# Kernel tuning notes

Measured on AMD Instinct MI355X. Metric: run time of the kernel, lower is better.

Reference implementation:

```python
import jax, jax.numpy as jnp
import numpy as np

B, S, M, H = 4, 512, 128, 768
KEY_SIZE, VALUE_SIZE = 30000, 10000


def setup_inputs() -> dict:
    key = jax.random.key(0)
    k1, k2, k3, k4, k5, k6 = jax.random.split(key, 6)
    return {
        "word_seq": jax.random.randint(k1, (B, M), 0, KEY_SIZE),
        "hidden_state": jax.random.normal(k2, (B, S, H), dtype=jnp.float32),
        "label_value_matrix": jax.random.randint(k3, (B, S, M), 0, VALUE_SIZE),
        "word_mask_metrix": jax.random.uniform(k4, (B, S, M), dtype=jnp.float32),
        "key_table": jax.random.normal(k5, (KEY_SIZE, H), dtype=jnp.float32) * 0.02,
        "value_table": jax.random.normal(k6, (VALUE_SIZE, H), dtype=jnp.float32) * 0.02,
    }


def reference(word_seq, hidden_state, label_value_matrix, word_mask_metrix,
              key_table, value_table):
    temper = jnp.asarray(H, hidden_state.dtype) ** 0.5
    emb_a = key_table[word_seq]                      # [B, M, H]
    # u[b,s,m] = <hidden_state[b,s], emb_a[b,m]> / sqrt(H)
    u = jnp.einsum('bsh,bmh->bsm', hidden_state, emb_a) / temper
    mask = jnp.clip(word_mask_metrix, 0.0, 1.0)      # [B, S, M]
    delta_exp_u = jnp.exp(u) * mask                  # masked unnormalized attn
    p = delta_exp_u / (jnp.sum(delta_exp_u, axis=2, keepdims=True) + 1e-10)
    emb_c = value_table[label_value_matrix]          # [B, S, M, H]
    # o[b,s,h] = sum_m p[b,s,m] * emb_c[b,s,m,h]
    o = jnp.einsum('bsm,bsmh->bsh', p, emb_c)
    return o
```

## Files before the change

### kernel.cpp

```cpp
#include <hip/hip_runtime.h>
#include <hip/hip_bf16.h>


constexpr int B = 4, S = 512, M = 128, H = 768;
constexpr int C4 = H / 4;
constexpr int KEY_SIZE = 30000, VALUE_SIZE = 10000;

constexpr int VT_N = VALUE_SIZE * H;
constexpr int KA_N = B * M * H;
constexpr int HS_N = B * S * H;
constexpr int U_N  = B * S * M;

constexpr size_t VT_BYTES = (size_t)VT_N * 2;
constexpr size_t KA_BYTES = (size_t)KA_N * 2;
constexpr size_t HS_BYTES = (size_t)HS_N * 2;
constexpr size_t U_BYTES  = (size_t)U_N  * 4;
constexpr size_t WS_NEEDED = VT_BYTES + KA_BYTES + HS_BYTES + U_BYTES;

constexpr int VT_V4 = VT_N / 4, KA_V4 = KA_N / 4, HS_V4 = HS_N / 4;
constexpr int CONV_TOTAL = VT_V4 + KA_V4 + HS_V4;

typedef short          bf16x8  __attribute__((ext_vector_type(8)));
typedef float          floatx4 __attribute__((ext_vector_type(4)));
typedef unsigned short ushort8v __attribute__((ext_vector_type(8)));

__device__ inline unsigned short f2bf(float f) {
    __hip_bfloat16 h = __float2bfloat16(f);
    return *reinterpret_cast<unsigned short*>(&h);
}
__device__ inline float bf2f(unsigned short u) {
    return __uint_as_float((unsigned)u << 16);
}
__device__ inline ushort4 f4_to_bf4(float4 f) {
    ushort4 u; u.x = f2bf(f.x); u.y = f2bf(f.y); u.z = f2bf(f.z); u.w = f2bf(f.w);
    return u;
}

__global__ __launch_bounds__(256) void convert_kernel(
    const float* __restrict__ vt, const float* __restrict__ kt,
    const float* __restrict__ hs, const int* __restrict__ wseq,
    unsigned short* __restrict__ vt_bf, unsigned short* __restrict__ ka_bf,
    unsigned short* __restrict__ hs_bf)
{
    int i = blockIdx.x * 256 + threadIdx.x;
    if (i < VT_V4) {
        ((ushort4*)vt_bf)[i] = f4_to_bf4(((const float4*)vt)[i]);
    } else if (i < VT_V4 + KA_V4) {
        int j   = i - VT_V4;
        int c   = j % (H / 4);
        int row = j / (H / 4);
        int src = wseq[row];
        float4 f = ((const float4*)(kt + (size_t)src * H))[c];
        ((ushort4*)ka_bf)[j] = f4_to_bf4(f);
    } else if (i < CONV_TOTAL) {
        int j = i - VT_V4 - KA_V4;
        ((ushort4*)hs_bf)[j] = f4_to_bf4(((const float4*)hs)[j]);
    }
}

__global__ __launch_bounds__(256) void phaseA_kernel(
    const unsigned short* __restrict__ hs_bf,
    const unsigned short* __restrict__ ka_bf,
    float* __restrict__ u_ws)
{
    const int lane = threadIdx.x & 63;
    const int wave = threadIdx.x >> 6;
    const int tile = blockIdx.x * 4 + wave;
    const int b    = tile >> 8;
    const int r    = tile & 255;
    const int s0   = (r >> 3) << 4;
    const int m0   = (r & 7) << 4;
    const int l15  = lane & 15;
    const int quad = lane >> 4;

    const unsigned short* arow = hs_bf + (size_t)(b * S + s0 + l15) * H + quad * 8;
    const unsigned short* brow = ka_bf + (size_t)(b * M + m0 + l15) * H + quad * 8;

    floatx4 acc = {0.f, 0.f, 0.f, 0.f};
    #pragma unroll 4
    for (int k = 0; k < H; k += 32) {
        bf16x8 af = *(const bf16x8*)(arow + k);
        bf16x8 bf = *(const bf16x8*)(brow + k);
        acc = __builtin_amdgcn_mfma_f32_16x16x32_bf16(af, bf, acc, 0, 0, 0);
    }
    float* up = u_ws + (size_t)(b * S + s0 + quad * 4) * M + m0 + l15;
    up[0 * M] = acc[0];
    up[1 * M] = acc[1];
    up[2 * M] = acc[2];
    up[3 * M] = acc[3];
}

__global__ __launch_bounds__(192) void gather_kernel(
    const float* __restrict__ u_ws,
    const int*   __restrict__ lvm,
    const float* __restrict__ mask,
    const unsigned short* __restrict__ vt_bf,
    float*       __restrict__ out)
{
    const int bs = blockIdx.x;
    const int t  = threadIdx.x;
    const int p  = t / 96;
    const int c  = t - p * 96;

    __shared__ float delta_s[M];
    __shared__ int   row_s[M];
    __shared__ float merge_s[8][100];
    __shared__ float dsum_s;

    const float inv_temper = rsqrtf((float)H);
    if (t < M) {
        float u  = u_ws[(size_t)bs * M + t];
        float mk = mask[(size_t)bs * M + t];
        mk = fminf(fmaxf(mk, 0.f), 1.f);
        delta_s[t] = __expf(u * inv_temper) * mk;
        row_s[t]   = lvm[(size_t)bs * M + t];
    }
    __syncthreads();

    if (t < 64) {
        float d = delta_s[t] + delta_s[t + 64];
        #pragma unroll
        for (int off = 1; off < 64; off <<= 1) d += __shfl_xor(d, off);
        if (t == 0) dsum_s = d + 1e-10f;
    }

    float a0 = 0.f, a1 = 0.f, a2 = 0.f, a3 = 0.f;
    float a4 = 0.f, a5 = 0.f, a6 = 0.f, a7 = 0.f;

    const unsigned short* base = vt_bf + c * 8;
    #pragma unroll 8
    for (int m = p; m < M; m += 2) {
        const float pm = delta_s[m];
        ushort8v v = *(const ushort8v*)(base + (size_t)row_s[m] * H);
        a0 += pm * bf2f(v[0]);
        a1 += pm * bf2f(v[1]);
        a2 += pm * bf2f(v[2]);
        a3 += pm * bf2f(v[3]);
        a4 += pm * bf2f(v[4]);
        a5 += pm * bf2f(v[5]);
        a6 += pm * bf2f(v[6]);
        a7 += pm * bf2f(v[7]);
    }

    if (p == 1) {
        merge_s[0][c] = a0; merge_s[1][c] = a1; merge_s[2][c] = a2; merge_s[3][c] = a3;
        merge_s[4][c] = a4; merge_s[5][c] = a5; merge_s[6][c] = a6; merge_s[7][c] = a7;
    }
    __syncthreads();

    if (p == 0) {
        const float inv_d = 1.0f / dsum_s;
        float4 r0, r1;
        r0.x = (a0 + merge_s[0][c]) * inv_d;
        r0.y = (a1 + merge_s[1][c]) * inv_d;
        r0.z = (a2 + merge_s[2][c]) * inv_d;
        r0.w = (a3 + merge_s[3][c]) * inv_d;
        r1.x = (a4 + merge_s[4][c]) * inv_d;
        r1.y = (a5 + merge_s[5][c]) * inv_d;
        r1.z = (a6 + merge_s[6][c]) * inv_d;
        r1.w = (a7 + merge_s[7][c]) * inv_d;
        float4* og = (float4*)(out + (size_t)bs * H + c * 8);
        og[0] = r0;
        og[1] = r1;
    }
}

__global__ __launch_bounds__(192) void kvmn_fp32_kernel(
    const int*   __restrict__ word_seq,
    const float* __restrict__ hidden_state,
    const int*   __restrict__ lvm,
    const float* __restrict__ mask,
    const float* __restrict__ key_table,
    const float* __restrict__ value_table,
    float*       __restrict__ out)
{
    const int bs   = blockIdx.x;
    const int b    = bs / S;
    const int t    = threadIdx.x;
    const int lane = t & 63;
    const int wave = t >> 6;

    __shared__ float4 hs4_s[C4];
    __shared__ int    wseq_s[M];
    __shared__ int    row_s[M];
    __shared__ float  mask_s[M];
    __shared__ float4 obuf[3][C4];
    __shared__ float  dsum_s3[3];

    const float4* hs_g4 = (const float4*)(hidden_state + (size_t)bs * H);
    hs4_s[t] = hs_g4[t];
    if (t < M) {
        wseq_s[t] = word_seq[b * M + t];
        row_s[t]  = lvm[(size_t)bs * M + t];
        float mk  = mask[(size_t)bs * M + t];
        mask_s[t] = fminf(fmaxf(mk, 0.f), 1.f);
    }
    __syncthreads();

    const float4 h0 = hs4_s[lane];
    const float4 h1 = hs4_s[lane + 64];
    const float4 h2 = hs4_s[lane + 128];
    const float inv_temper = rsqrtf((float)H);
    const float4* kt4 = (const float4*)key_table;
    const float4* vt4 = (const float4*)value_table;

    float4 a0 = {0.f,0.f,0.f,0.f}, a1 = {0.f,0.f,0.f,0.f}, a2 = {0.f,0.f,0.f,0.f};
    float dsum = 0.f;

    #pragma unroll 2
    for (int m = wave; m < M; m += 3) {
        const float4* kr = kt4 + (size_t)wseq_s[m] * C4;
        const float4* vr = vt4 + (size_t)row_s[m]  * C4;
        const float4 k0 = kr[lane], k1 = kr[lane+64], k2 = kr[lane+128];
        const float4 v0 = vr[lane], v1 = vr[lane+64], v2 = vr[lane+128];
        float dot = h0.x*k0.x + h0.y*k0.y + h0.z*k0.z + h0.w*k0.w
                  + h1.x*k1.x + h1.y*k1.y + h1.z*k1.z + h1.w*k1.w
                  + h2.x*k2.x + h2.y*k2.y + h2.z*k2.z + h2.w*k2.w;
        #pragma unroll
        for (int off = 1; off < 64; off <<= 1) dot += __shfl_xor(dot, off);
        const float delta = __expf(dot * inv_temper) * mask_s[m];
        dsum += delta;
        a0.x += delta*v0.x; a0.y += delta*v0.y; a0.z += delta*v0.z; a0.w += delta*v0.w;
        a1.x += delta*v1.x; a1.y += delta*v1.y; a1.z += delta*v1.z; a1.w += delta*v1.w;
        a2.x += delta*v2.x; a2.y += delta*v2.y; a2.z += delta*v2.z; a2.w += delta*v2.w;
    }
    obuf[wave][lane] = a0; obuf[wave][lane+64] = a1; obuf[wave][lane+128] = a2;
    if (lane == 0) dsum_s3[wave] = dsum;
    __syncthreads();
    const float inv_d = 1.0f / (dsum_s3[0] + dsum_s3[1] + dsum_s3[2] + 1e-10f);
    const float4 r0 = obuf[0][t], r1 = obuf[1][t], r2 = obuf[2][t];
    float4 r;
    r.x = (r0.x+r1.x+r2.x)*inv_d; r.y = (r0.y+r1.y+r2.y)*inv_d;
    r.z = (r0.z+r1.z+r2.z)*inv_d; r.w = (r0.w+r1.w+r2.w)*inv_d;
    ((float4*)(out + (size_t)bs * H))[t] = r;
}

extern "C" void kernel_launch(void* const* d_in, const int* in_sizes, int n_in,
                              void* d_out, int out_size, void* d_ws, size_t ws_size,
                              hipStream_t stream) {
    const int*   word_seq    = (const int*)  d_in[0];
    const float* hidden      = (const float*)d_in[1];
    const int*   lvm         = (const int*)  d_in[2];
    const float* mask        = (const float*)d_in[3];
    const float* key_table   = (const float*)d_in[4];
    const float* value_table = (const float*)d_in[5];
    float* out = (float*)d_out;

    if (ws_size >= WS_NEEDED) {
        unsigned short* vt_bf = (unsigned short*)d_ws;
        unsigned short* ka_bf = (unsigned short*)((char*)d_ws + VT_BYTES);
        unsigned short* hs_bf = (unsigned short*)((char*)d_ws + VT_BYTES + KA_BYTES);
        float*          u_ws  = (float*)((char*)d_ws + VT_BYTES + KA_BYTES + HS_BYTES);

        convert_kernel<<<(CONV_TOTAL + 255) / 256, 256, 0, stream>>>(
            value_table, key_table, hidden, word_seq, vt_bf, ka_bf, hs_bf);
        phaseA_kernel<<<(B * S / 16) * (M / 16) / 4, 256, 0, stream>>>(
            hs_bf, ka_bf, u_ws);
        gather_kernel<<<B * S, 192, 0, stream>>>(
            u_ws, lvm, mask, vt_bf, out);
    } else {
        kvmn_fp32_kernel<<<B * S, 192, 0, stream>>>(
            word_seq, hidden, lvm, mask, key_table, value_table, out);
    }
}
```

Baseline: 203.9 us.

## Fuse bf16 conversion and QK MFMA into one prep kernel

Merges the conversion kernel and the score-GEMM kernel into a single launch. 64 blocks compute the hidden·key scores with MFMA, reading fp32 hidden state and gathering key-table rows directly and converting to bf16 in registers. The remaining blocks convert the value table to bf16. This removes one launch and the bf16 staging buffers for the hidden state and gathered keys. In exchange, the GEMM runs on only 64 blocks, four tiles per wave, with each fp32 operand reread once per tile rather than from a compact bf16 copy.

```diff
diff --git a/kernel.cpp b/kernel.cpp
--- a/kernel.cpp
+++ b/kernel.cpp
@@ -7,21 +7,19 @@
 constexpr int KEY_SIZE = 30000, VALUE_SIZE = 10000;
 
 constexpr int VT_N = VALUE_SIZE * H;
-constexpr int KA_N = B * M * H;
-constexpr int HS_N = B * S * H;
 constexpr int U_N  = B * S * M;
 
 constexpr size_t VT_BYTES = (size_t)VT_N * 2;
-constexpr size_t KA_BYTES = (size_t)KA_N * 2;
-constexpr size_t HS_BYTES = (size_t)HS_N * 2;
 constexpr size_t U_BYTES  = (size_t)U_N  * 4;
-constexpr size_t WS_NEEDED = VT_BYTES + KA_BYTES + HS_BYTES + U_BYTES;
-
-constexpr int VT_V4 = VT_N / 4, KA_V4 = KA_N / 4, HS_V4 = HS_N / 4;
-constexpr int CONV_TOTAL = VT_V4 + KA_V4 + HS_V4;
-
-typedef short          bf16x8  __attribute__((ext_vector_type(8)));
-typedef float          floatx4 __attribute__((ext_vector_type(4)));
+constexpr size_t WS_NEEDED = VT_BYTES + U_BYTES;
+
+constexpr int VT_V4      = VT_N / 4;
+constexpr int NB_PHASEA  = 64;
+constexpr int NB_VT      = VT_V4 / 256;
+constexpr int NB_PREP    = NB_PHASEA + NB_VT;
+
+typedef short          bf16x8   __attribute__((ext_vector_type(8)));
+typedef float          floatx4  __attribute__((ext_vector_type(4)));
 typedef unsigned short ushort8v __attribute__((ext_vector_type(8)));
 
 __device__ inline unsigned short f2bf(float f) {
@@ -35,59 +33,66 @@
     ushort4 u; u.x = f2bf(f.x); u.y = f2bf(f.y); u.z = f2bf(f.z); u.w = f2bf(f.w);
     return u;
 }
-
-__global__ __launch_bounds__(256) void convert_kernel(
-    const float* __restrict__ vt, const float* __restrict__ kt,
-    const float* __restrict__ hs, const int* __restrict__ wseq,
-    unsigned short* __restrict__ vt_bf, unsigned short* __restrict__ ka_bf,
-    unsigned short* __restrict__ hs_bf)
+__device__ inline bf16x8 f8_to_bf8(float4 a, float4 b) {
+    bf16x8 r;
+    r[0] = (short)f2bf(a.x); r[1] = (short)f2bf(a.y);
+    r[2] = (short)f2bf(a.z); r[3] = (short)f2bf(a.w);
+    r[4] = (short)f2bf(b.x); r[5] = (short)f2bf(b.y);
+    r[6] = (short)f2bf(b.z); r[7] = (short)f2bf(b.w);
+    return r;
+}
+
+__global__ __launch_bounds__(256) void prep_kernel(
+    const float* __restrict__ vt,
+    const float* __restrict__ kt,
+    const float* __restrict__ hs,
+    const int*   __restrict__ wseq,
+    unsigned short* __restrict__ vt_bf,
+    float*       __restrict__ u_ws)
 {
-    int i = blockIdx.x * 256 + threadIdx.x;
-    if (i < VT_V4) {
+    if (blockIdx.x >= NB_PHASEA) {
+        int i = (blockIdx.x - NB_PHASEA) * 256 + threadIdx.x;
         ((ushort4*)vt_bf)[i] = f4_to_bf4(((const float4*)vt)[i]);
-    } else if (i < VT_V4 + KA_V4) {
-        int j   = i - VT_V4;
-        int c   = j % (H / 4);
-        int row = j / (H / 4);
-        int src = wseq[row];
-        float4 f = ((const float4*)(kt + (size_t)src * H))[c];
-        ((ushort4*)ka_bf)[j] = f4_to_bf4(f);
-    } else if (i < CONV_TOTAL) {
-        int j = i - VT_V4 - KA_V4;
-        ((ushort4*)hs_bf)[j] = f4_to_bf4(((const float4*)hs)[j]);
-    }
-}
-
-__global__ __launch_bounds__(256) void phaseA_kernel(
-    const unsigned short* __restrict__ hs_bf,
-    const unsigned short* __restrict__ ka_bf,
-    float* __restrict__ u_ws)
-{
+        return;
+    }
+
     const int lane = threadIdx.x & 63;
     const int wave = threadIdx.x >> 6;
     const int tile = blockIdx.x * 4 + wave;
-    const int b    = tile >> 8;
-    const int r    = tile & 255;
+    const int b    = tile >> 6;
+    const int r    = tile & 63;
     const int s0   = (r >> 3) << 4;
-    const int m0   = (r & 7) << 4;
-    const int l15  = lane & 15;
-    const int quad = lane >> 4;
-
-    const unsigned short* arow = hs_bf + (size_t)(b * S + s0 + l15) * H + quad * 8;
-    const unsigned short* brow = ka_bf + (size_t)(b * M + m0 + l15) * H + quad * 8;
-
-    floatx4 acc = {0.f, 0.f, 0.f, 0.f};
-    #pragma unroll 4
-    for (int k = 0; k < H; k += 32) {
-        bf16x8 af = *(const bf16x8*)(arow + k);
-        bf16x8 bf = *(const bf16x8*)(brow + k);
-        acc = __builtin_amdgcn_mfma_f32_16x16x32_bf16(af, bf, acc, 0, 0, 0);
-    }
-    float* up = u_ws + (size_t)(b * S + s0 + quad * 4) * M + m0 + l15;
-    up[0 * M] = acc[0];
-    up[1 * M] = acc[1];
-    up[2 * M] = acc[2];
-    up[3 * M] = acc[3];
+    (void)b; (void)r; (void)s0;
+
+    const float inv_one = 1.0f; (void)inv_one;
+    for (int rep = 0; rep < 4; ++rep) {
+        const int tid  = tile + rep * 256;
+        const int bb   = tid >> 8;
+        const int rr   = tid & 255;
+        const int ss0  = (rr >> 3) << 4;
+        const int mm0  = (rr & 7) << 4;
+        const int l15  = lane & 15;
+        const int quad = lane >> 4;
+
+        const float* arow = hs + (size_t)(bb * S + ss0 + l15) * H + quad * 8;
+        const int    krow = wseq[bb * M + mm0 + l15];
+        const float* brow = kt + (size_t)krow * H + quad * 8;
+
+        floatx4 acc = {0.f, 0.f, 0.f, 0.f};
+        #pragma unroll 4
+        for (int k = 0; k < H; k += 32) {
+            const float4* ap = (const float4*)(arow + k);
+            const float4* bp = (const float4*)(brow + k);
+            bf16x8 af = f8_to_bf8(ap[0], ap[1]);
+            bf16x8 bf = f8_to_bf8(bp[0], bp[1]);
+            acc = __builtin_amdgcn_mfma_f32_16x16x32_bf16(af, bf, acc, 0, 0, 0);
+        }
+        float* up = u_ws + (size_t)(bb * S + ss0 + quad * 4) * M + mm0 + l15;
+        up[0 * M] = acc[0];
+        up[1 * M] = acc[1];
+        up[2 * M] = acc[2];
+        up[3 * M] = acc[3];
+    }
 }
 
 __global__ __launch_bounds__(192) void gather_kernel(
@@ -248,14 +253,10 @@
 
     if (ws_size >= WS_NEEDED) {
         unsigned short* vt_bf = (unsigned short*)d_ws;
-        unsigned short* ka_bf = (unsigned short*)((char*)d_ws + VT_BYTES);
-        unsigned short* hs_bf = (unsigned short*)((char*)d_ws + VT_BYTES + KA_BYTES);
-        float*          u_ws  = (float*)((char*)d_ws + VT_BYTES + KA_BYTES + HS_BYTES);
-
-        convert_kernel<<<(CONV_TOTAL + 255) / 256, 256, 0, stream>>>(
-            value_table, key_table, hidden, word_seq, vt_bf, ka_bf, hs_bf);
-        phaseA_kernel<<<(B * S / 16) * (M / 16) / 4, 256, 0, stream>>>(
-            hs_bf, ka_bf, u_ws);
+        float*          u_ws  = (float*)((char*)d_ws + VT_BYTES);
+
+        prep_kernel<<<NB_PREP, 256, 0, stream>>>(
+            value_table, key_table, hidden, word_seq, vt_bf, u_ws);
         gather_kernel<<<B * S, 192, 0, stream>>>(
             u_ws, lvm, mask, vt_bf, out);
     } else {
```

After: 229.7 us. 1.13x slower.
